# Kernel optimization log

Measured on AMD Instinct MI355X. Metric: run time of the kernel, lower is better.

The kernel has to match this reference:

```python
import jax, jax.numpy as jnp
import numpy as np

N_TOKENS, OUT, E, H, D = 32, 1, 768, 12, 8
B, L = 64, 256
DH = E // H


def layer_norm(x, g, b, eps=1e-5):
    mu = jnp.mean(x, axis=-1, keepdims=True)
    var = jnp.mean((x - mu) ** 2, axis=-1, keepdims=True)
    return (x - mu) * jax.lax.rsqrt(var + eps) * g + b


def setup_inputs() -> dict:
    key = jax.random.key(0)
    ks = jax.random.split(key, 16)
    tokens = jax.random.randint(ks[0], (B, L), 0, N_TOKENS)
    padding = jnp.zeros((B, L), dtype=bool)
    r = jax.random.normal(ks[1], (B, L, 3), dtype=jnp.float32) * 3.0
    s = 0.02
    embed = jax.random.normal(ks[2], (N_TOKENS, E), jnp.float32) * s
    embed = embed.at[0].set(0.0)  # padding_idx=0
    inp = dict(
        tokens=tokens, padding=padding, r=r, embed=embed,
        mu=jax.random.uniform(ks[3], (D, H), jnp.float32, 0.0, 4.0),
        gamma=jax.random.uniform(ks[4], (D, H), jnp.float32, 0.1, 1.0),
        w=jax.random.normal(ks[5], (D, H), jnp.float32),
        Wqkv=jax.random.normal(ks[6], (D, E, 3 * E), jnp.float32) * s,
        bqkv=jnp.zeros((D, 3 * E), jnp.float32),
        Wo=jax.random.normal(ks[7], (D, E, E), jnp.float32) * s,
        bo=jnp.zeros((D, E), jnp.float32),
        ln1_g=jnp.ones((D, E), jnp.float32), ln1_b=jnp.zeros((D, E), jnp.float32),
        W1=jax.random.normal(ks[8], (D, E, 4 * E), jnp.float32) * s,
        b1=jnp.zeros((D, 4 * E), jnp.float32),
        W2=jax.random.normal(ks[9], (D, 4 * E, E), jnp.float32) * s,
        b2=jnp.zeros((D, E), jnp.float32),
        ln2_g=jnp.ones((D, E), jnp.float32), ln2_b=jnp.zeros((D, E), jnp.float32),
        lnf_g=jnp.ones((E,), jnp.float32), lnf_b=jnp.zeros((E,), jnp.float32),
        Wout=jax.random.normal(ks[10], (E, OUT), jnp.float32) * s,
        bout=jnp.zeros((OUT,), jnp.float32),
    )
    return inp


def reference(tokens, padding, r, embed, mu, gamma, w, Wqkv, bqkv, Wo, bo,
              ln1_g, ln1_b, W1, b1, W2, b2, ln2_g, ln2_b, lnf_g, lnf_b, Wout, bout):
    Bc, Lc = tokens.shape
    # pairwise distances (eps for grad stability at d=0 on diagonal)
    diff = r[:, :, None, :] - r[:, None, :, :]              # [B,L,L,3]
    d = jnp.sqrt(jnp.sum(diff * diff, axis=-1) + 1e-12)     # [B,L,L]
    diag = jnp.eye(Lc, dtype=bool)
    pad_pair = padding[:, None, :] | padding[:, :, None]    # [B,L,L]
    attn_mask = (pad_pair | diag)[:, None, :, :]            # [B,1,L,L] True=blocked
    pad_e = padding[:, :, None]                              # [B,L,1]
    neg = jnp.asarray(-1e9, jnp.float32)

    e = embed[tokens]                                        # [B,L,E]
    scale = 1.0 / np.sqrt(DH)
    for i in range(D):
        # learned per-head Gaussian RBF attention bias
        bias = w[i][None, :, None, None] * jnp.exp(
            -gamma[i][None, :, None, None] * (d[:, None, :, :] - mu[i][None, :, None, None]) ** 2
        )                                                    # [B,H,L,L]
        e0 = layer_norm(e, ln1_g[i], ln1_b[i])
        qkv = e0 @ Wqkv[i] + bqkv[i]
        q, k, v = jnp.split(qkv, 3, axis=-1)
        q = q.reshape(Bc, Lc, H, DH).transpose(0, 2, 1, 3)
        k = k.reshape(Bc, Lc, H, DH).transpose(0, 2, 1, 3)
        v = v.reshape(Bc, Lc, H, DH).transpose(0, 2, 1, 3)
        scores = jnp.einsum('bhid,bhjd->bhij', q, k) * scale + bias
        scores = jnp.where(attn_mask, neg, scores)
        a = jax.nn.softmax(scores, axis=-1)
        o = jnp.einsum('bhij,bhjd->bhid', a, v)
        o = o.transpose(0, 2, 1, 3).reshape(Bc, Lc, E)
        e1 = o @ Wo[i] + bo[i]
        e2 = layer_norm(e1 + e0, ln2_g[i], ln2_b[i])
        e3 = jax.nn.relu(e2 @ W1[i] + b1[i]) @ W2[i] + b2[i]
        e3 = jnp.where(pad_e, 0.0, e3)
        e = e3 + e2
    e = layer_norm(e, lnf_g, lnf_b)
    e = jnp.mean(e, axis=1)
    return e @ Wout + bout
```

## Files before the change

kernel.cpp:

```cpp
#include <hip/hip_runtime.h>
#include <cstdint>
#include <cstddef>

#define B_    64
#define L_    256
#define E_    768
#define H_    12
#define DH_   64
#define D_    8
#define FF_   3072
#define QKV3_ 2304
#define M_    (B_*L_)

typedef _Float16 f16;
typedef f16   f16x8  __attribute__((ext_vector_type(8)));
typedef float f32x4  __attribute__((ext_vector_type(4)));

__device__ __forceinline__ void gl_lds16(const void* g, void* l){
    __builtin_amdgcn_global_load_lds(
        (const __attribute__((address_space(1))) void*)g,
        (__attribute__((address_space(3))) void*)l, 16, 0, 0);
}

__global__ void sentinel_kernel(float* out, int n){
    int i = blockIdx.x*64 + threadIdx.x;
    if (i < n) out[i] = 1.0e6f;
}

__global__ __launch_bounds__(256) void gather_kernel(
    const int* __restrict__ tok, const float* __restrict__ emb, float* __restrict__ e)
{
    const int idx = blockIdx.x*256 + threadIdx.x;
    const int row = idx / E_;
    const int d   = idx - row*E_;
    e[idx] = emb[(size_t)tok[row]*E_ + d];
}

__global__ void wsplit_kernel(const float* __restrict__ W, f16* __restrict__ Hh, int K, int N)
{
    __shared__ float tile[32][33];
    const int tx = threadIdx.x, ty = threadIdx.y;
#pragma unroll
    for (int i2 = 0; i2 < 4; ++i2){
        const int k = blockIdx.y*32 + ty + i2*8;
        const int n = blockIdx.x*32 + tx;
        tile[ty + i2*8][tx] = W[(size_t)k*N + n];
    }
    __syncthreads();
    const int k2 = blockIdx.y*32 + tx;
#pragma unroll
    for (int i2 = 0; i2 < 4; ++i2){
        const int n2 = blockIdx.x*32 + ty + i2*8;
        Hh[(size_t)n2*K + k2] = (f16)tile[tx][ty + i2*8];
    }
}

__global__ __launch_bounds__(256) void ln_kernel(
    const float* __restrict__ x, const float* __restrict__ g, const float* __restrict__ bb,
    float* __restrict__ yF, f16* __restrict__ yH, f16* __restrict__ yL)
{
    __shared__ float red[256];
    const int row = blockIdx.x, tid = threadIdx.x;
    const float* xr = x + (size_t)row*E_;
    float v0 = xr[tid], v1 = xr[tid+256], v2 = xr[tid+512];
    red[tid] = v0 + v1 + v2;
    __syncthreads();
    for (int o = 128; o; o >>= 1){ if (tid < o) red[tid] += red[tid+o]; __syncthreads(); }
    const float mean = red[0] * (1.f/768.f);
    __syncthreads();
    const float d0 = v0-mean, d1 = v1-mean, d2 = v2-mean;
    red[tid] = d0*d0 + d1*d1 + d2*d2;
    __syncthreads();
    for (int o = 128; o; o >>= 1){ if (tid < o) red[tid] += red[tid+o]; __syncthreads(); }
    const float rstd = rsqrtf(red[0]*(1.f/768.f) + 1e-5f);
    const float dv[3] = {d0, d1, d2};
#pragma unroll
    for (int q = 0; q < 3; ++q){
        const int d = tid + q*256;
        const float y = dv[q]*rstd*g[d] + bb[d];
        const size_t idx = (size_t)row*E_ + d;
        if (yF) yF[idx] = y;
        if (yH){
            const f16 hi = (f16)y;
            yH[idx] = hi;
            yL[idx] = (f16)(y - (float)hi);
        }
    }
}

template<int MODE>
__global__ __launch_bounds__(256, 4) void gemm_kernel(
    const f16* __restrict__ A, const f16* __restrict__ Bh,
    const float* __restrict__ bias,
    const f16* __restrict__ exH, const f16* __restrict__ exL,
    const unsigned char* __restrict__ pad,
    float* __restrict__ Cf, f16* __restrict__ Cq,
    f16* __restrict__ qh, f16* __restrict__ kh, f16* __restrict__ vt,
    int Mn, int Nn, int Kn)
{
    __shared__ f16 sA0[128*32];
    __shared__ f16 sA1[128*32];
    __shared__ f16 sB0[128*32];
    __shared__ f16 sB1[128*32];
    const int tid = threadIdx.x;
    const int w = tid >> 6, l = tid & 63;
    const int nt = gridDim.x;
    const int flat = blockIdx.y * nt + blockIdx.x;
    const int xcd = flat & 7, grp = flat >> 3;
    const int bx = grp % nt;
    const int by = xcd + 8 * (grp / nt);
    const int m0 = by * 128, n0 = bx * 128;
    const int waveM = (w & 1) * 64, waveN = (w >> 1) * 64;
    const int fr = l & 15, fq = l >> 4;
    f32x4 acc[4][4] = {};

    const int e0i = tid * 8;
    const int r0  = e0i >> 5, k0o = e0i & 31;
    const int e1i = e0i + 2048;
    const int r1  = e1i >> 5, k1o = e1i & 31;

    const f16* pa0 = A  + (size_t)(m0 + r0) * Kn + k0o;
    const f16* pa1 = A  + (size_t)(m0 + r1) * Kn + k1o;
    const f16* pb0 = Bh + (size_t)(n0 + r0) * Kn + k0o;
    const f16* pb1 = Bh + (size_t)(n0 + r1) * Kn + k1o;

#define STAGE_(SA, SB, KK) do { \
        gl_lds16(pa0 + (KK), &SA[e0i]); \
        gl_lds16(pa1 + (KK), &SA[e1i]); \
        gl_lds16(pb0 + (KK), &SB[e0i]); \
        gl_lds16(pb1 + (KK), &SB[e1i]); \
    } while(0)

#define COMPUTE_(SA, SB) do { \
        f16x8 fa[4], fb[4]; \
        _Pragma("unroll") \
        for (int i = 0; i < 4; ++i){ \
            fa[i] = *(const f16x8*)&SA[(waveM + i*16 + fr)*32 + fq*8]; \
            fb[i] = *(const f16x8*)&SB[(waveN + i*16 + fr)*32 + fq*8]; \
        } \
        _Pragma("unroll") \
        for (int i = 0; i < 4; ++i) \
        _Pragma("unroll") \
        for (int j = 0; j < 4; ++j) \
            acc[i][j] = __builtin_amdgcn_mfma_f32_16x16x32_f16(fa[i], fb[j], acc[i][j], 0,0,0); \
    } while(0)

    const int nsteps = Kn >> 5;
    STAGE_(sA0, sB0, 0);
    __syncthreads();
    for (int s = 0; s < nsteps; s += 2){
        STAGE_(sA1, sB1, (s+1)*32);
        COMPUTE_(sA0, sB0);
        __syncthreads();
        const bool more = (s + 2 < nsteps);
        if (more) STAGE_(sA0, sB0, (s+2)*32);
        COMPUTE_(sA1, sB1);
        if (more) __syncthreads();
    }
#undef STAGE_
#undef COMPUTE_

#pragma unroll
    for (int jt = 0; jt < 4; ++jt){
        const int col = n0 + waveN + jt*16 + fr;
        const float bc = bias[col];
        int which = 0, hh = 0, dd = 0;
        if (MODE == 0){
            which = col / 768;
            const int hc = col - which*768;
            hh = hc >> 6; dd = hc & 63;
        }
#pragma unroll
        for (int it = 0; it < 4; ++it)
#pragma unroll
            for (int rg = 0; rg < 4; ++rg){
                const int row = m0 + waveM + it*16 + fq*4 + rg;
                float v = acc[it][jt][rg] + bc;
                if (MODE == 0){
                    const int bb2 = row >> 8, jj2 = row & 255;
                    const size_t bh = (size_t)bb2 * H_ + hh;
                    if (which == 0)      qh[(bh*256 + jj2)*64 + dd] = (f16)v;
                    else if (which == 1) kh[(bh*256 + jj2)*64 + dd] = (f16)v;
                    else                 vt[(bh*64 + dd)*256 + jj2] = (f16)v;
                } else {
                    const size_t idx = (size_t)row * Nn + col;
                    if (MODE == 1){
                        Cf[idx] = v + (float)exH[idx] + (float)exL[idx];
                    } else if (MODE == 2){
                        Cq[idx] = (f16)fmaxf(v, 0.f);
                    } else {
                        if (pad[row]) v = 0.f;
                        Cf[idx] = v + (float)exH[idx] + (float)exL[idx];
                    }
                }
            }
    }
}

__global__ __launch_bounds__(256, 4) void attn_kernel(
    const f16* __restrict__ qh, const f16* __restrict__ kh, const f16* __restrict__ vt,
    const float* __restrict__ rpos, const unsigned char* __restrict__ pad,
    const float* __restrict__ mu, const float* __restrict__ ga, const float* __restrict__ wv,
    f16* __restrict__ o)
{
    __shared__ f16 sK[64*72];
    __shared__ f16 sV[64*72];
    __shared__ f16 sP[4][16*72];
    __shared__ float rx[256], ry[256], rz[256], pf[256];

    const int h = blockIdx.x, b = blockIdx.y, p = blockIdx.z;
    const int tid = threadIdx.x, w = tid >> 6, l = tid & 63;
    const int fr = l & 15, fq = l >> 4;
    const float muh = mu[h], gah = ga[h], wh = wv[h];
    const size_t bh = (size_t)b * H_ + h;
    const int rowbase = b * L_;

    rx[tid] = rpos[(size_t)(rowbase+tid)*3 + 0];
    ry[tid] = rpos[(size_t)(rowbase+tid)*3 + 1];
    rz[tid] = rpos[(size_t)(rowbase+tid)*3 + 2];
    pf[tid] = pad[rowbase+tid] ? 1.f : 0.f;

    f16x8 fQ[2];
    {
        const int r = p*64 + w*16 + fr;
        const f16* qp = qh + (bh*256 + r)*64 + fq*8;
        fQ[0] = *(const f16x8*)(qp);
        fQ[1] = *(const f16x8*)(qp + 32);
    }

    float m_[4], l_[4];
    f32x4 oacc[4] = {};
#pragma unroll
    for (int rg = 0; rg < 4; ++rg){ m_[rg] = -3.0e38f; l_[rg] = 0.f; }
    __syncthreads();

    for (int c = 0; c < 4; ++c){
        __syncthreads();
        {
            const int e0 = tid*8, e1 = e0 + 2048;
            const int kr0 = e0 >> 6, kd0 = e0 & 63;
            const int kr1 = e1 >> 6, kd1 = e1 & 63;
            *(uint4*)&sK[kr0*72 + kd0] = *(const uint4*)&kh[(bh*256 + c*64 + kr0)*64 + kd0];
            *(uint4*)&sK[kr1*72 + kd1] = *(const uint4*)&kh[(bh*256 + c*64 + kr1)*64 + kd1];
            *(uint4*)&sV[kr0*72 + kd0] = *(const uint4*)&vt[(bh*64 + kr0)*256 + c*64 + kd0];
            *(uint4*)&sV[kr1*72 + kd1] = *(const uint4*)&vt[(bh*64 + kr1)*256 + c*64 + kd1];
        }
        __syncthreads();
        f32x4 sacc[4] = {};
#pragma unroll
        for (int nt = 0; nt < 4; ++nt)
#pragma unroll
            for (int kf = 0; kf < 2; ++kf){
                const f16x8 fb = *(const f16x8*)&sK[(nt*16 + fr)*72 + kf*32 + fq*8];
                sacc[nt] = __builtin_amdgcn_mfma_f32_16x16x32_f16(fQ[kf], fb, sacc[nt], 0,0,0);
            }
        float sv[4][4];
        float rmax[4] = {-3.0e38f, -3.0e38f, -3.0e38f, -3.0e38f};
        const int ibase = p*64 + w*16 + fq*4;
#pragma unroll
        for (int nt = 0; nt < 4; ++nt){
            const int j = c*64 + nt*16 + fr;
            const float jx = rx[j], jy = ry[j], jz = rz[j], jp = pf[j];
#pragma unroll
            for (int rg = 0; rg < 4; ++rg){
                const int i = ibase + rg;
                const float dx = rx[i]-jx, dy = ry[i]-jy, dz = rz[i]-jz;
                const float dist = sqrtf(dx*dx + dy*dy + dz*dz + 1e-12f);
                const float t = dist - muh;
                float s = sacc[nt][rg]*0.125f + wh*__expf(-gah*t*t);
                if ((j == i) | (pf[i] != 0.f) | (jp != 0.f)) s = -1e9f;
                sv[nt][rg] = s;
                rmax[rg] = fmaxf(rmax[rg], s);
            }
        }
#pragma unroll
        for (int rg = 0; rg < 4; ++rg){
#pragma unroll
            for (int off = 8; off >= 1; off >>= 1)
                rmax[rg] = fmaxf(rmax[rg], __shfl_xor(rmax[rg], off));
            const float mnew = fmaxf(m_[rg], rmax[rg]);
            const float alpha = __expf(m_[rg] - mnew);
            m_[rg] = mnew;
            l_[rg] *= alpha;
#pragma unroll
            for (int dt = 0; dt < 4; ++dt) oacc[dt][rg] *= alpha;
            float rs = 0.f;
#pragma unroll
            for (int nt = 0; nt < 4; ++nt){
                const float pv = __expf(sv[nt][rg] - mnew);
                sP[w][(fq*4 + rg)*72 + nt*16 + fr] = (f16)pv;
                rs += pv;
            }
#pragma unroll
            for (int off = 8; off >= 1; off >>= 1) rs += __shfl_xor(rs, off);
            l_[rg] += rs;
        }
#pragma unroll
        for (int kf = 0; kf < 2; ++kf){
            const f16x8 pa = *(const f16x8*)&sP[w][fr*72 + kf*32 + fq*8];
#pragma unroll
            for (int dt = 0; dt < 4; ++dt){
                const f16x8 vb = *(const f16x8*)&sV[(dt*16 + fr)*72 + kf*32 + fq*8];
                oacc[dt] = __builtin_amdgcn_mfma_f32_16x16x32_f16(pa, vb, oacc[dt], 0,0,0);
            }
        }
    }
    const int rglob = rowbase + p*64 + w*16 + fq*4;
#pragma unroll
    for (int rg = 0; rg < 4; ++rg){
        const float inv = 1.f / l_[rg];
#pragma unroll
        for (int dt = 0; dt < 4; ++dt)
            o[(size_t)(rglob + rg)*E_ + h*64 + dt*16 + fr] = (f16)(oacc[dt][rg]*inv);
    }
}

__global__ __launch_bounds__(256) void mean_kernel(const float* __restrict__ x, float* __restrict__ m)
{
    const int b = blockIdx.x, tid = threadIdx.x;
    const float* xb = x + (size_t)b*L_*E_;
#pragma unroll
    for (int q = 0; q < 3; ++q){
        const int d = tid + q*256;
        float s = 0.f;
        for (int l2 = 0; l2 < L_; ++l2) s += xb[(size_t)l2*E_ + d];
        m[b*E_ + d] = s * (1.f/(float)L_);
    }
}

__global__ __launch_bounds__(256) void out_kernel(
    const float* __restrict__ m, const float* __restrict__ Wout,
    const float* __restrict__ bout, float* __restrict__ out)
{
    __shared__ float red[256];
    const int b = blockIdx.x, tid = threadIdx.x;
    float s = 0.f;
#pragma unroll
    for (int q = 0; q < 3; ++q){ const int d = tid + q*256; s += m[b*E_ + d]*Wout[d]; }
    red[tid] = s;
    __syncthreads();
    for (int o = 128; o; o >>= 1){ if (tid < o) red[tid] += red[tid+o]; __syncthreads(); }
    if (tid == 0) out[b] = red[0] + bout[0];
}

extern "C" void kernel_launch(void* const* d_in, const int* in_sizes, int n_in,
                              void* d_out, int out_size, void* d_ws, size_t ws_size,
                              hipStream_t stream)
{
    const int*            tokens  = (const int*)d_in[0];
    const unsigned char*  padding = (const unsigned char*)d_in[1];
    const float*          rpos    = (const float*)d_in[2];
    const float*          embed   = (const float*)d_in[3];
    const float*          mu      = (const float*)d_in[4];
    const float*          ga      = (const float*)d_in[5];
    const float*          wv      = (const float*)d_in[6];
    const float*          Wqkv    = (const float*)d_in[7];
    const float*          bqkv    = (const float*)d_in[8];
    const float*          Wo      = (const float*)d_in[9];
    const float*          bo      = (const float*)d_in[10];
    const float*          ln1g    = (const float*)d_in[11];
    const float*          ln1b    = (const float*)d_in[12];
    const float*          W1      = (const float*)d_in[13];
    const float*          b1      = (const float*)d_in[14];
    const float*          W2      = (const float*)d_in[15];
    const float*          b2      = (const float*)d_in[16];
    const float*          ln2g    = (const float*)d_in[17];
    const float*          ln2b    = (const float*)d_in[18];
    const float*          lnfg    = (const float*)d_in[19];
    const float*          lnfb    = (const float*)d_in[20];
    const float*          Wout    = (const float*)d_in[21];
    const float*          bout    = (const float*)d_in[22];
    float* out = (float*)d_out;
    (void)in_sizes; (void)n_in;

    char* ws = (char*)d_ws;
    size_t off = 0;
    auto alloc = [&](size_t bytes)->char*{
        char* p = ws + off;
        off += (bytes + 255) & ~(size_t)255;
        return p;
    };
    const size_t PLANE = (size_t)M_*E_;
    float* e     = (float*)alloc(PLANE*4);
    char*  big   = alloc(PLANE*2*4);
    f16*   actH  = (f16*)alloc(PLANE*2);
    f16*   actL  = (f16*)alloc(PLANE*2);
    f16*   wqh   = (f16*)alloc((size_t)E_*QKV3_*2);
    f16*   woh   = (f16*)alloc((size_t)E_*E_*2);
    f16*   w1h   = (f16*)alloc((size_t)E_*FF_*2);
    f16*   w2h   = (f16*)alloc((size_t)FF_*E_*2);
    float* meanb = (float*)alloc((size_t)B_*E_*4);
    const size_t required = off;

    if (ws_size < required){
        sentinel_kernel<<<dim3((out_size+63)/64), dim3(64), 0, stream>>>(out, out_size);
        return;
    }

    f16*   qh   = (f16*)big;
    f16*   kh   = qh + PLANE;
    f16*   vt   = kh + PLANE;
    f16*   ob   = vt + PLANE;
    f16*   hbuf = (f16*)big;
    float* lnfo = (float*)big;
    float* sbuf = e;

    gather_kernel<<<dim3(M_*E_/256), dim3(256), 0, stream>>>(tokens, embed, e);

    for (int i = 0; i < D_; ++i){
        wsplit_kernel<<<dim3(QKV3_/32, E_/32), dim3(32,8), 0, stream>>>(
            Wqkv + (size_t)i*E_*QKV3_, wqh, E_, QKV3_);
        wsplit_kernel<<<dim3(E_/32, E_/32), dim3(32,8), 0, stream>>>(
            Wo + (size_t)i*E_*E_, woh, E_, E_);
        wsplit_kernel<<<dim3(FF_/32, E_/32), dim3(32,8), 0, stream>>>(
            W1 + (size_t)i*E_*FF_, w1h, E_, FF_);
        wsplit_kernel<<<dim3(E_/32, FF_/32), dim3(32,8), 0, stream>>>(
            W2 + (size_t)i*FF_*E_, w2h, FF_, E_);

        ln_kernel<<<dim3(M_), dim3(256), 0, stream>>>(e, ln1g + i*E_, ln1b + i*E_, nullptr, actH, actL);
        gemm_kernel<0><<<dim3(QKV3_/128, M_/128), dim3(256), 0, stream>>>(
            actH, wqh, bqkv + i*QKV3_, nullptr, nullptr, nullptr,
            nullptr, nullptr, qh, kh, vt, M_, QKV3_, E_);
        attn_kernel<<<dim3(H_, B_, 4), dim3(256), 0, stream>>>(
            qh, kh, vt, rpos, padding, mu + i*H_, ga + i*H_, wv + i*H_, ob);
        gemm_kernel<1><<<dim3(E_/128, M_/128), dim3(256), 0, stream>>>(
            ob, woh, bo + i*E_, actH, actL, nullptr,
            sbuf, nullptr, nullptr, nullptr, nullptr, M_, E_, E_);
        ln_kernel<<<dim3(M_), dim3(256), 0, stream>>>(sbuf, ln2g + i*E_, ln2b + i*E_, nullptr, actH, actL);
        gemm_kernel<2><<<dim3(FF_/128, M_/128), dim3(256), 0, stream>>>(
            actH, w1h, b1 + i*FF_, nullptr, nullptr, nullptr,
            nullptr, hbuf, nullptr, nullptr, nullptr, M_, FF_, E_);
        gemm_kernel<3><<<dim3(E_/128, M_/128), dim3(256), 0, stream>>>(
            hbuf, w2h, b2 + i*E_, actH, actL, padding,
            e, nullptr, nullptr, nullptr, nullptr, M_, E_, FF_);
    }

    ln_kernel<<<dim3(M_), dim3(256), 0, stream>>>(e, lnfg, lnfb, lnfo, nullptr, nullptr);
    mean_kernel<<<dim3(B_), dim3(256), 0, stream>>>(lnfo, meanb);
    out_kernel<<<dim3(B_), dim3(256), 0, stream>>>(meanb, Wout, bout, out);
}
```

Measured before the change: 4.724 ms.

## Deepen GEMM LDS pipeline to four stages with explicit vmcnt waits

Replaces the two-buffer LDS double buffering in the GEMM kernel with a four-buffer ring that keeps three K-tiles of global-to-LDS loads in flight. It uses explicit s_waitcnt vmcnt counts and raw barriers, and raises wave priority around the MFMA block. The aim is to hide global memory latency better across K steps. The cost is twice the LDS per block (64 KB), so launch bounds drop to 2 blocks per CU, which lowers occupancy. It also adds two barriers per K step.

```diff
diff --git a/kernel.cpp b/kernel.cpp
--- a/kernel.cpp
+++ b/kernel.cpp
@@ -89,7 +89,7 @@
 }
 
 template<int MODE>
-__global__ __launch_bounds__(256, 4) void gemm_kernel(
+__global__ __launch_bounds__(256, 2) void gemm_kernel(
     const f16* __restrict__ A, const f16* __restrict__ Bh,
     const float* __restrict__ bias,
     const f16* __restrict__ exH, const f16* __restrict__ exL,
@@ -98,10 +98,8 @@
     f16* __restrict__ qh, f16* __restrict__ kh, f16* __restrict__ vt,
     int Mn, int Nn, int Kn)
 {
-    __shared__ f16 sA0[128*32];
-    __shared__ f16 sA1[128*32];
-    __shared__ f16 sB0[128*32];
-    __shared__ f16 sB1[128*32];
+    __shared__ f16 sA[4][128*32];
+    __shared__ f16 sB[4][128*32];
     const int tid = threadIdx.x;
     const int w = tid >> 6, l = tid & 63;
     const int nt = gridDim.x;
@@ -124,41 +122,60 @@
     const f16* pb0 = Bh + (size_t)(n0 + r0) * Kn + k0o;
     const f16* pb1 = Bh + (size_t)(n0 + r1) * Kn + k1o;
 
-#define STAGE_(SA, SB, KK) do { \
-        gl_lds16(pa0 + (KK), &SA[e0i]); \
-        gl_lds16(pa1 + (KK), &SA[e1i]); \
-        gl_lds16(pb0 + (KK), &SB[e0i]); \
-        gl_lds16(pb1 + (KK), &SB[e1i]); \
+#define STAGE_(U, KK) do { \
+        const size_t ko_ = (size_t)(KK) * 32; \
+        gl_lds16(pa0 + ko_, &sA[U][e0i]); \
+        gl_lds16(pa1 + ko_, &sA[U][e1i]); \
+        gl_lds16(pb0 + ko_, &sB[U][e0i]); \
+        gl_lds16(pb1 + ko_, &sB[U][e1i]); \
     } while(0)
 
-#define COMPUTE_(SA, SB) do { \
+#define COMPUTE_(U) do { \
         f16x8 fa[4], fb[4]; \
         _Pragma("unroll") \
         for (int i = 0; i < 4; ++i){ \
-            fa[i] = *(const f16x8*)&SA[(waveM + i*16 + fr)*32 + fq*8]; \
-            fb[i] = *(const f16x8*)&SB[(waveN + i*16 + fr)*32 + fq*8]; \
+            fa[i] = *(const f16x8*)&sA[U][(waveM + i*16 + fr)*32 + fq*8]; \
+            fb[i] = *(const f16x8*)&sB[U][(waveN + i*16 + fr)*32 + fq*8]; \
         } \
+        __builtin_amdgcn_s_setprio(1); \
         _Pragma("unroll") \
         for (int i = 0; i < 4; ++i) \
         _Pragma("unroll") \
         for (int j = 0; j < 4; ++j) \
             acc[i][j] = __builtin_amdgcn_mfma_f32_16x16x32_f16(fa[i], fb[j], acc[i][j], 0,0,0); \
+        __builtin_amdgcn_s_setprio(0); \
     } while(0)
 
+#define WAITV12 asm volatile("s_waitcnt vmcnt(12)" ::: "memory")
+#define WAITV8  asm volatile("s_waitcnt vmcnt(8)"  ::: "memory")
+#define WAITV4  asm volatile("s_waitcnt vmcnt(4)"  ::: "memory")
+#define WAITV0  asm volatile("s_waitcnt vmcnt(0)"  ::: "memory")
+#define BAR_    do { asm volatile("" ::: "memory"); __builtin_amdgcn_s_barrier(); asm volatile("" ::: "memory"); } while(0)
+
     const int nsteps = Kn >> 5;
-    STAGE_(sA0, sB0, 0);
-    __syncthreads();
-    for (int s = 0; s < nsteps; s += 2){
-        STAGE_(sA1, sB1, (s+1)*32);
-        COMPUTE_(sA0, sB0);
-        __syncthreads();
-        const bool more = (s + 2 < nsteps);
-        if (more) STAGE_(sA0, sB0, (s+2)*32);
-        COMPUTE_(sA1, sB1);
-        if (more) __syncthreads();
+    STAGE_(0, 0);
+    STAGE_(1, 1);
+    STAGE_(2, 2);
+    for (int s = 0; s < nsteps; s += 4){
+#pragma unroll
+        for (int u = 0; u < 4; ++u){
+            const int st = s + u;
+            if (st + 3 < nsteps){ STAGE_((u+3)&3, st+3); WAITV12; }
+            else if (st + 2 < nsteps){ WAITV8; }
+            else if (st + 1 < nsteps){ WAITV4; }
+            else { WAITV0; }
+            BAR_;
+            COMPUTE_(u);
+            BAR_;
+        }
     }
 #undef STAGE_
 #undef COMPUTE_
+#undef WAITV12
+#undef WAITV8
+#undef WAITV4
+#undef WAITV0
+#undef BAR_
 
 #pragma unroll
     for (int jt = 0; jt < 4; ++jt){
```

Result: no change. 4.720 ms (-0.1%).
